# Kernel optimization log

Measured on AMD Instinct MI355X. Metric: run time of the kernel, lower is better.

## Reference

```python
import jax, jax.numpy as jnp
import numpy as np

N_NODES = 100000
N_EDGES = 1600000


def setup_inputs() -> dict:
    key = jax.random.key(0)
    ks = jax.random.split(key, 16)
    d_emb, d_mlp, d_lstm = 128, 256, 256
    B, C, T = 8, 4, 128
    return {
        "input_ids": jax.random.randint(ks[0], (B, C, T), 0, N_NODES, dtype=jnp.int64 if jax.config.jax_enable_x64 else jnp.int32),
        "input_mask": jnp.ones((B, C, T), dtype=jnp.int32),
        "labels": jax.random.uniform(ks[1], (B, C), dtype=jnp.float32),
        "src": jax.random.randint(ks[2], (N_EDGES,), 0, N_NODES),
        "dst": jax.random.randint(ks[3], (N_EDGES,), 0, N_NODES),
        "edge_value": jax.random.uniform(ks[4], (N_EDGES,), dtype=jnp.float32),
        "node_emb": jax.random.normal(ks[5], (N_NODES, d_emb), dtype=jnp.float32),
        "W1": jax.random.normal(ks[6], (d_mlp, d_emb), dtype=jnp.float32) * 0.05,
        "b1": jax.random.normal(ks[7], (d_mlp,), dtype=jnp.float32) * 0.05,
        "w_ih": jax.random.normal(ks[8], (4 * d_lstm, d_mlp), dtype=jnp.float32) * 0.05,
        "w_hh": jax.random.normal(ks[9], (4 * d_lstm, d_lstm), dtype=jnp.float32) * 0.05,
        "b_ih": jax.random.normal(ks[10], (4 * d_lstm,), dtype=jnp.float32) * 0.05,
        "b_hh": jax.random.normal(ks[11], (4 * d_lstm,), dtype=jnp.float32) * 0.05,
        "W2": jax.random.normal(ks[12], (1, d_lstm), dtype=jnp.float32) * 0.05,
        "b2": jax.random.normal(ks[13], (1,), dtype=jnp.float32) * 0.05,
    }


def reference(input_ids, input_mask, labels, src, dst, edge_value,
              node_emb, W1, b1, w_ih, w_hh, b_ih, b_hh, W2, b2):
    N = node_emb.shape[0]
    # edge-weighted mean message passing: u_mul_e('embedding','value') -> mean
    m = node_emb[src] * edge_value[:, None]                       # [E, d_emb]
    agg = jax.ops.segment_sum(m, dst, num_segments=N)             # [N, d_emb]
    cnt = jax.ops.segment_sum(jnp.ones_like(edge_value), dst, num_segments=N)
    h_nodes = agg / jnp.maximum(cnt, 1.0)[:, None]
    # linear1 on all nodes
    t_nodes = h_nodes @ W1.T + b1                                  # [N, d_mlp]
    B, C, T = input_ids.shape
    x = t_nodes[input_ids.reshape(B * C, T)]                       # [BC, T, d_mlp]
    lengths = input_mask.sum(axis=-1).reshape(B * C)               # [BC]
    H = w_hh.shape[1]

    def step(carry, xt):
        h, c = carry
        gates = xt @ w_ih.T + b_ih + h @ w_hh.T + b_hh
        i, f, g, o = jnp.split(gates, 4, axis=-1)  # torch LSTM gate order
        c = jax.nn.sigmoid(f) * c + jax.nn.sigmoid(i) * jnp.tanh(g)
        h = jax.nn.sigmoid(o) * jnp.tanh(c)
        return (h, c), h

    h0 = jnp.zeros((B * C, H), x.dtype)
    _, hs = jax.lax.scan(step, (h0, h0), jnp.swapaxes(x, 0, 1))    # [T, BC, H]
    hs = jnp.swapaxes(hs, 0, 1)                                    # [BC, T, H]
    idx = (lengths - 1).astype(jnp.int32)[:, None, None]
    h_last = jnp.take_along_axis(hs, jnp.broadcast_to(idx, (B * C, 1, H)), axis=1)[:, 0, :]
    scores = (h_last @ W2.T + b2).reshape(B, C)                    # [B, 4]
    p = jax.nn.softmax(scores, axis=1)
    # BCEWithLogits applied to softmaxed scores (as in the original)
    error = jnp.mean(jnp.maximum(p, 0) - p * labels + jnp.log1p(jnp.exp(-jnp.abs(p))))
    predictions = jnp.argmax(p, axis=1)
    return error, predictions
```

## Files before the change

### kernel.cpp

```cpp
#include <hip/hip_runtime.h>
#include <math.h>

#define NNODES 100000
#define NEDGES 1600000
#define NPOS   4096
#define NSEQ   32
#define TSTEPS 128

typedef float f32x4 __attribute__((ext_vector_type(4)));
typedef unsigned u32x4 __attribute__((ext_vector_type(4)));
typedef _Float16 h2v __attribute__((ext_vector_type(2)));

#define OFF_SLOT   0
#define OFF_AGG    400128
#define OFF_CNT    2497280
#define OFF_WF     2513664
#define OFF_BIASF  3037952
#define OFF_PREG   3042048
#define OFF_HS     19819264
#define OFF_WH16A  OFF_AGG
#define OFF_WH16L  (OFF_AGG + 192 * 512 * 4)

static __device__ __forceinline__ float fdot2(unsigned w, unsigned h, float acc) {
#if __has_builtin(__builtin_amdgcn_fdot2)
  h2v wv, hv;
  __builtin_memcpy(&wv, &w, 4);
  __builtin_memcpy(&hv, &h, 4);
  return __builtin_amdgcn_fdot2(wv, hv, acc, false);
#else
  asm("v_dot2_f32_f16 %0, %1, %2, %0" : "+v"(acc) : "v"(w), "v"(h));
  return acc;
#endif
}

__global__ void k_init(int* slotmap, float* agg, float* cnt, float* hs0) {
  int i = blockIdx.x * blockDim.x + threadIdx.x;
  int stride = gridDim.x * blockDim.x;
  for (int idx = i; idx < 4096 * 128; idx += stride) agg[idx] = 0.f;
  for (int idx = i; idx < NNODES; idx += stride) slotmap[idx] = -1;
  for (int idx = i; idx < 4096; idx += stride) cnt[idx] = 0.f;
  for (int idx = i; idx < 8192; idx += stride) hs0[idx] = 0.f;
}

__global__ void k_mark(const int* __restrict__ input_ids, int* __restrict__ slotmap) {
  int p = blockIdx.x * blockDim.x + threadIdx.x;
  if (p < NPOS) atomicCAS(&slotmap[input_ids[p]], -1, p);
}

__global__ void k_edge(const int* __restrict__ src, const int* __restrict__ dst,
                       const float* __restrict__ ev, const float* __restrict__ emb,
                       const int* __restrict__ slotmap,
                       float* __restrict__ agg, float* __restrict__ cnt) {
  int e = blockIdx.x * 256 + threadIdx.x;
  int lane = threadIdx.x & 63;
  int d = dst[e];
  int slot = slotmap[d];
  int sn = 0; float vv = 0.f;
  if (slot >= 0) { sn = src[e]; vv = ev[e]; }
  unsigned long long m = __ballot(slot >= 0);
  while (m) {
    int j = __ffsll(m) - 1;
    m &= m - 1;
    int sl = __shfl(slot, j);
    int s2 = __shfl(sn, j);
    float v = __shfl(vv, j);
    float2 em = *(const float2*)&emb[(size_t)s2 * 128 + 2 * lane];
    atomicAdd(&agg[sl * 128 + 2 * lane],     em.x * v);
    atomicAdd(&agg[sl * 128 + 2 * lane + 1], em.y * v);
    if (lane == 0) atomicAdd(&cnt[sl], 1.f);
  }
}

__global__ void k_div(float* __restrict__ agg, const float* __restrict__ cnt) {
  int i = blockIdx.x * blockDim.x + threadIdx.x;
  agg[i] /= fmaxf(cnt[i >> 7], 1.f);
}

__global__ void k_fuse(const float* __restrict__ w_ih, const float* __restrict__ W1,
                       const float* __restrict__ b1, const float* __restrict__ b_ih,
                       const float* __restrict__ b_hh,
                       float* __restrict__ Wf, float* __restrict__ bf) {
  int row = blockIdx.x;
  int e = threadIdx.x;
  float acc = 0.f;
  for (int m2 = 0; m2 < 256; ++m2) acc += w_ih[row * 256 + m2] * W1[m2 * 128 + e];
  Wf[row * 128 + e] = acc;
  if (e == 0) {
    float bacc = b_ih[row] + b_hh[row];
    for (int m2 = 0; m2 < 256; ++m2) bacc += w_ih[row * 256 + m2] * b1[m2];
    bf[row] = bacc;
  }
}

__global__ __launch_bounds__(256, 2) void k_pregemm(
    const float* __restrict__ hnode, const float* __restrict__ Wf,
    const float* __restrict__ bf, const int* __restrict__ slotmap,
    const int* __restrict__ input_ids, float* __restrict__ preg) {
  __shared__ float Ash[64][132];
  __shared__ float Bsh[64][132];
  __shared__ int slots[64];
  int tid = threadIdx.x;
  int bm = (blockIdx.x & 63) * 64;
  int bn = (blockIdx.x >> 6) * 64;
  if (tid < 64) slots[tid] = slotmap[input_ids[bm + tid]];
  __syncthreads();
#pragma unroll
  for (int i = 0; i < 8; ++i) {
    int idx = tid + 256 * i;
    int r = idx >> 5, c = idx & 31;
    *(float4*)&Ash[r][c * 4] = *(const float4*)&hnode[slots[r] * 128 + c * 4];
    *(float4*)&Bsh[r][c * 4] = *(const float4*)&Wf[(bn + r) * 128 + c * 4];
  }
  __syncthreads();
  int tx = tid & 15, ty = tid >> 4;
  float acc[4][4] = {};
  for (int k = 0; k < 128; k += 4) {
    float4 a[4], bb[4];
#pragma unroll
    for (int i = 0; i < 4; ++i) a[i] = *(const float4*)&Ash[tx + 16 * i][k];
#pragma unroll
    for (int j = 0; j < 4; ++j) bb[j] = *(const float4*)&Bsh[ty + 16 * j][k];
#pragma unroll
    for (int i = 0; i < 4; ++i)
#pragma unroll
      for (int j = 0; j < 4; ++j)
        acc[i][j] += a[i].x * bb[j].x + a[i].y * bb[j].y + a[i].z * bb[j].z + a[i].w * bb[j].w;
  }
#pragma unroll
  for (int j = 0; j < 4; ++j) {
    int row = bn + ty + 16 * j;
    float bias = bf[row];
    int q  = row >> 8;
    int mm = (row >> 5) & 7;
    int dl = row & 31;
#pragma unroll
    for (int i = 0; i < 4; ++i) {
      int p = bm + tx + 16 * i;
      int s = p >> 7, tt = p & 127;
      preg[(((size_t)(tt * 32 + s) * 8 + mm) * 4 + q) * 32 + dl] = acc[i][j] + bias;
    }
  }
}

__global__ void k_wcvt(const float* __restrict__ w_hh,
                       unsigned* __restrict__ wA, unsigned* __restrict__ wL) {
  int idx = blockIdx.x * 256 + threadIdx.x;
  int row = idx >> 7;
  int j   = idx & 127;
  float x0 = w_hh[(size_t)row * 256 + 2 * j];
  float x1 = w_hh[(size_t)row * 256 + 2 * j + 1];
  union { _Float16 f[2]; unsigned u; } pk;
  pk.f[0] = (_Float16)x0;
  pk.f[1] = (_Float16)x1;
  int q = row >> 8, d = row & 255;
  int kseg = j >> 6, jj = j & 63;
  int tid = kseg * 256 + d;
  if (q < 3) {
    wA[(q * 64 + jj) * 512 + tid] = pk.u;
  } else {
    wL[((jj >> 2) * 512 + tid) * 4 + (jj & 3)] = pk.u;
  }
}

__global__ __launch_bounds__(512) void k_lstm(
    const unsigned* __restrict__ wh16A, const unsigned* __restrict__ wh16L,
    const float* __restrict__ preg, float* __restrict__ hs) {
  __shared__ __align__(16) unsigned whL[16 * 512 * 4];
  __shared__ __align__(16) unsigned h16[128];
  __shared__ __align__(16) float    accb[256 * 4];
  const int tid  = threadIdx.x;
  const int s    = blockIdx.x;
  const int kseg = tid >> 8;
  const int d    = tid & 255;
  const bool owner = (kseg == 0);

  unsigned wv[192];
  {
    const unsigned* wa = wh16A + tid;
#pragma unroll
    for (int e = 0; e < 192; ++e) wv[e] = wa[e * 512];
#pragma unroll
    for (int i = 0; i < 16; ++i)
      *(u32x4*)&whL[(i * 512 + tid) * 4] = *(const u32x4*)&wh16L[(i * 512 + tid) * 4];
  }
  if (tid < 128) h16[tid] = 0u;
  float c_st = 0.f;
  __syncthreads();

  const float* pregs = preg + ((size_t)s * 8 + (d >> 5)) * 128 + (d & 31);

  for (int t = 0; t < TSTEPS; ++t) {
    float pg0 = 0.f, pg1 = 0.f, pg2 = 0.f, pg3 = 0.f;
    if (owner) {
      const float* pb = pregs + (size_t)t * 32768;
      pg0 = pb[0]; pg1 = pb[32]; pg2 = pb[64]; pg3 = pb[96];
    }
    float a0 = 0.f, a1 = 0.f, a2 = 0.f, a3 = 0.f;
    const unsigned* hseg = h16 + kseg * 64;
#pragma unroll
    for (int c = 0; c < 16; ++c) {
      u32x4 h4 = *(const u32x4*)(hseg + c * 4);
      u32x4 w3 = *(const u32x4*)&whL[(c * 512 + tid) * 4];
#pragma unroll
      for (int k = 0; k < 4; ++k) {
        a0 = fdot2(wv[0 * 64 + c * 4 + k], h4[k], a0);
        a1 = fdot2(wv[1 * 64 + c * 4 + k], h4[k], a1);
        a2 = fdot2(wv[2 * 64 + c * 4 + k], h4[k], a2);
        a3 = fdot2(w3[k],                  h4[k], a3);
      }
    }
    if (!owner) {
      f32x4 r; r.x = a0; r.y = a1; r.z = a2; r.w = a3;
      *(f32x4*)&accb[d * 4] = r;
    }
    __syncthreads();
    if (owner) {
      f32x4 r = *(const f32x4*)&accb[d * 4];
      float gi = a0 + r.x + pg0;
      float gf = a1 + r.y + pg1;
      float gg = a2 + r.z + pg2;
      float go = a3 + r.w + pg3;
      float si = 1.f / (1.f + expf(-gi));
      float sf = 1.f / (1.f + expf(-gf));
      float so = 1.f / (1.f + expf(-go));
      float cc = sf * c_st + si * tanhf(gg);
      float hh = so * tanhf(cc);
      c_st = cc;
      ((_Float16*)h16)[d] = (_Float16)hh;
      hs[(size_t)(t + 1) * 8192 + s * 256 + d] = hh;
    }
    __syncthreads();
  }
}

__global__ void k_final(const float* __restrict__ hs, const int* __restrict__ mask,
                        const float* __restrict__ labels, const float* __restrict__ W2,
                        const float* __restrict__ b2, float* __restrict__ out) {
  __shared__ float scores[32];
  __shared__ float errpart[8];
  int tid = threadIdx.x;
  if (tid < 32) {
    int len = 0;
    for (int t = 0; t < 128; ++t) len += mask[tid * 128 + t];
    if (len < 1) len = 1;
    const float* hl = hs + (size_t)len * 8192 + tid * 256;
    float acc = b2[0];
    for (int k = 0; k < 256; ++k) acc += hl[k] * W2[k];
    scores[tid] = acc;
  }
  __syncthreads();
  if (tid < 8) {
    float sc[4];
#pragma unroll
    for (int i = 0; i < 4; ++i) sc[i] = scores[tid * 4 + i];
    float mx = fmaxf(fmaxf(sc[0], sc[1]), fmaxf(sc[2], sc[3]));
    float ex[4], ssum = 0.f;
#pragma unroll
    for (int i = 0; i < 4; ++i) { ex[i] = expf(sc[i] - mx); ssum += ex[i]; }
    float esum = 0.f; int am = 0; float best = -1e30f;
#pragma unroll
    for (int i = 0; i < 4; ++i) {
      float p = ex[i] / ssum;
      float li = labels[tid * 4 + i];
      esum += fmaxf(p, 0.f) - p * li + log1pf(expf(-fabsf(p)));
      if (p > best) { best = p; am = i; }
    }
    errpart[tid] = esum;
    out[1 + tid] = (float)am;
  }
  __syncthreads();
  if (tid == 0) {
    float e = 0.f;
    for (int i = 0; i < 8; ++i) e += errpart[i];
    out[0] = e / 32.f;
  }
}

extern "C" void kernel_launch(void* const* d_in, const int* in_sizes, int n_in,
                              void* d_out, int out_size, void* d_ws, size_t ws_size,
                              hipStream_t stream) {
  const int*   input_ids  = (const int*)d_in[0];
  const int*   input_mask = (const int*)d_in[1];
  const float* labels     = (const float*)d_in[2];
  const int*   src        = (const int*)d_in[3];
  const int*   dst        = (const int*)d_in[4];
  const float* ev         = (const float*)d_in[5];
  const float* node_emb   = (const float*)d_in[6];
  const float* W1         = (const float*)d_in[7];
  const float* b1         = (const float*)d_in[8];
  const float* w_ih       = (const float*)d_in[9];
  const float* w_hh       = (const float*)d_in[10];
  const float* b_ih       = (const float*)d_in[11];
  const float* b_hh       = (const float*)d_in[12];
  const float* W2         = (const float*)d_in[13];
  const float* b2         = (const float*)d_in[14];
  float* out = (float*)d_out;
  char* ws = (char*)d_ws;
  int*      slotmap = (int*)(ws + OFF_SLOT);
  float*    agg     = (float*)(ws + OFF_AGG);
  float*    cnt     = (float*)(ws + OFF_CNT);
  float*    Wf      = (float*)(ws + OFF_WF);
  float*    biasf   = (float*)(ws + OFF_BIASF);
  float*    preg    = (float*)(ws + OFF_PREG);
  float*    hs      = (float*)(ws + OFF_HS);
  unsigned* wh16A   = (unsigned*)(ws + OFF_WH16A);
  unsigned* wh16L   = (unsigned*)(ws + OFF_WH16L);

  hipLaunchKernelGGL(k_init,    dim3(2048), dim3(256), 0, stream, slotmap, agg, cnt, hs);
  hipLaunchKernelGGL(k_mark,    dim3(16),   dim3(256), 0, stream, input_ids, slotmap);
  hipLaunchKernelGGL(k_edge,    dim3(6250), dim3(256), 0, stream, src, dst, ev, node_emb, slotmap, agg, cnt);
  hipLaunchKernelGGL(k_div,     dim3(2048), dim3(256), 0, stream, agg, cnt);
  hipLaunchKernelGGL(k_fuse,    dim3(1024), dim3(128), 0, stream, w_ih, W1, b1, b_ih, b_hh, Wf, biasf);
  hipLaunchKernelGGL(k_pregemm, dim3(1024), dim3(256), 0, stream, agg, Wf, biasf, slotmap, input_ids, preg);
  hipLaunchKernelGGL(k_wcvt,    dim3(512),  dim3(256), 0, stream, w_hh, wh16A, wh16L);
  hipLaunchKernelGGL(k_lstm,    dim3(NSEQ), dim3(512), 0, stream, wh16A, wh16L, preg, hs);
  hipLaunchKernelGGL(k_final,   dim3(1),    dim3(64),  0, stream, hs, input_mask, labels, W2, b2, out);
}
```

Measured before the change: 338.0 us.

## Repartition LSTM recurrence: two outputs per thread, four K-segments, weights split across registers/LDS/global

The recurrent LSTM kernel now has each thread compute gates for two hidden units over a quarter of the K dimension, instead of one unit over half of K. The fp16 w_hh is split three ways: a register-resident part (16 u32x4), an LDS part (18 chunks) and a part streamed from global/L2 each step (wS). The point is to cut per-step dot-product latency on the serial critical path and to spread the weight storage over the available storage levels. In exchange it adds global loads on every timestep, a three-way partial-sum reduction through LDS, and a complicated weight-layout conversion that could be wrong.

Result: slower. 381.0 us (+12.7%).

```diff
diff --git a/kernel.cpp b/kernel.cpp
--- a/kernel.cpp
+++ b/kernel.cpp
@@ -18,8 +18,9 @@
 #define OFF_BIASF  3037952
 #define OFF_PREG   3042048
 #define OFF_HS     19819264
-#define OFF_WH16A  OFF_AGG
-#define OFF_WH16L  (OFF_AGG + 192 * 512 * 4)
+#define OFF_WR  OFF_AGG
+#define OFF_WL  (OFF_AGG + 131072)
+#define OFF_WS  (OFF_AGG + 131072 + 147456)
 
 static __device__ __forceinline__ float fdot2(unsigned w, unsigned h, float acc) {
 #if __has_builtin(__builtin_amdgcn_fdot2)
@@ -31,6 +32,14 @@
   asm("v_dot2_f32_f16 %0, %1, %2, %0" : "+v"(acc) : "v"(w), "v"(h));
   return acc;
 #endif
+}
+
+static __device__ __forceinline__ float dotq(u32x4 w, u32x4 h, float a) {
+  a = fdot2(w[0], h[0], a);
+  a = fdot2(w[1], h[1], a);
+  a = fdot2(w[2], h[2], a);
+  a = fdot2(w[3], h[3], a);
+  return a;
 }
 
 __global__ void k_init(int* slotmap, float* agg, float* cnt, float* hs0) {
@@ -142,8 +151,8 @@
   }
 }
 
-__global__ void k_wcvt(const float* __restrict__ w_hh,
-                       unsigned* __restrict__ wA, unsigned* __restrict__ wL) {
+__global__ void k_wcvt(const float* __restrict__ w_hh, unsigned* __restrict__ wR,
+                       unsigned* __restrict__ wL, unsigned* __restrict__ wS) {
   int idx = blockIdx.x * 256 + threadIdx.x;
   int row = idx >> 7;
   int j   = idx & 127;
@@ -152,82 +161,153 @@
   union { _Float16 f[2]; unsigned u; } pk;
   pk.f[0] = (_Float16)x0;
   pk.f[1] = (_Float16)x1;
-  int q = row >> 8, d = row & 255;
-  int kseg = j >> 6, jj = j & 63;
-  int tid = kseg * 256 + d;
-  if (q < 3) {
-    wA[(q * 64 + jj) * 512 + tid] = pk.u;
+  int q = row >> 8, dout = row & 255;
+  int dim2 = dout & 1, dd2 = dout >> 1;
+  int r = dim2 * 4 + q;
+  int kseg = j >> 5, p = j & 31;
+  int b = p >> 4, i = (p >> 2) & 3, lane = p & 3;
+  int tid = kseg * 128 + dd2;
+  if (r < 2) {
+    int qr = (b * 2 + r) * 4 + i;
+    wR[(qr * 4 + lane) * 512 + tid] = pk.u;
+  } else if (b == 0 && (r == 3 || r == 4)) {
+    wL[(((r - 3) * 4 + i) * 512 + tid) * 4 + lane] = pk.u;
+  } else if (b == 1 && r == 2) {
+    wL[((8 + i) * 512 + tid) * 4 + lane] = pk.u;
+  } else if (b == 1 && r == 3) {
+    wL[((12 + i) * 512 + tid) * 4 + lane] = pk.u;
+  } else if (b == 1 && r == 4 && i < 2) {
+    wL[((16 + i) * 512 + tid) * 4 + lane] = pk.u;
+  } else if (b == 0 && r == 2) {
+    wS[(i * 512 + tid) * 4 + lane] = pk.u;
+  } else if (b == 0) {
+    wS[((4 + (r - 5) * 4 + i) * 512 + tid) * 4 + lane] = pk.u;
+  } else if (r == 4) {
+    wS[((16 + (i - 2)) * 512 + tid) * 4 + lane] = pk.u;
   } else {
-    wL[((jj >> 2) * 512 + tid) * 4 + (jj & 3)] = pk.u;
+    wS[((18 + (r - 5) * 4 + i) * 512 + tid) * 4 + lane] = pk.u;
   }
 }
 
 __global__ __launch_bounds__(512) void k_lstm(
-    const unsigned* __restrict__ wh16A, const unsigned* __restrict__ wh16L,
-    const float* __restrict__ preg, float* __restrict__ hs) {
-  __shared__ __align__(16) unsigned whL[16 * 512 * 4];
+    const unsigned* __restrict__ wR, const unsigned* __restrict__ wL,
+    const unsigned* __restrict__ wS, const float* __restrict__ preg,
+    float* __restrict__ hs) {
+  __shared__ __align__(16) unsigned whL[18 * 512 * 4];
   __shared__ __align__(16) unsigned h16[128];
-  __shared__ __align__(16) float    accb[256 * 4];
-  const int tid  = threadIdx.x;
-  const int s    = blockIdx.x;
-  const int kseg = tid >> 8;
-  const int d    = tid & 255;
+  __shared__ __align__(16) float    accb[3 * 128 * 8];
+  const int tid = threadIdx.x;
+  const int s = blockIdx.x;
+  const int kseg = tid >> 7;
+  const int dd2 = tid & 127;
   const bool owner = (kseg == 0);
 
-  unsigned wv[192];
+  u32x4 rq[16];
+#pragma unroll
+  for (int qr = 0; qr < 16; ++qr)
+#pragma unroll
+    for (int l = 0; l < 4; ++l)
+      rq[qr][l] = wR[(qr * 4 + l) * 512 + tid];
   {
-    const unsigned* wa = wh16A + tid;
-#pragma unroll
-    for (int e = 0; e < 192; ++e) wv[e] = wa[e * 512];
-#pragma unroll
-    for (int i = 0; i < 16; ++i)
-      *(u32x4*)&whL[(i * 512 + tid) * 4] = *(const u32x4*)&wh16L[(i * 512 + tid) * 4];
+    const u32x4* src = (const u32x4*)wL;
+    u32x4* dst = (u32x4*)whL;
+#pragma unroll
+    for (int lc = 0; lc < 18; ++lc)
+      dst[lc * 512 + tid] = src[lc * 512 + tid];
   }
   if (tid < 128) h16[tid] = 0u;
-  float c_st = 0.f;
-  __syncthreads();
-
-  const float* pregs = preg + ((size_t)s * 8 + (d >> 5)) * 128 + (d & 31);
+  float c0s = 0.f, c1s = 0.f;
+  __syncthreads();
+
+  const u32x4* hqp = (const u32x4*)h16 + kseg * 8;
+  const u32x4* lq = (const u32x4*)whL;
+  const u32x4* sq = (const u32x4*)wS;
 
   for (int t = 0; t < TSTEPS; ++t) {
-    float pg0 = 0.f, pg1 = 0.f, pg2 = 0.f, pg3 = 0.f;
+    float2 pg0, pg1, pg2, pg3;
     if (owner) {
-      const float* pb = pregs + (size_t)t * 32768;
-      pg0 = pb[0]; pg1 = pb[32]; pg2 = pb[64]; pg3 = pb[96];
+      const float* pb = preg + (((size_t)(t * 32 + s) * 8 + (dd2 >> 4)) * 4) * 32
+                        + ((2 * dd2) & 31);
+      pg0 = *(const float2*)&pb[0];
+      pg1 = *(const float2*)&pb[32];
+      pg2 = *(const float2*)&pb[64];
+      pg3 = *(const float2*)&pb[96];
     }
     float a0 = 0.f, a1 = 0.f, a2 = 0.f, a3 = 0.f;
-    const unsigned* hseg = h16 + kseg * 64;
-#pragma unroll
-    for (int c = 0; c < 16; ++c) {
-      u32x4 h4 = *(const u32x4*)(hseg + c * 4);
-      u32x4 w3 = *(const u32x4*)&whL[(c * 512 + tid) * 4];
-#pragma unroll
-      for (int k = 0; k < 4; ++k) {
-        a0 = fdot2(wv[0 * 64 + c * 4 + k], h4[k], a0);
-        a1 = fdot2(wv[1 * 64 + c * 4 + k], h4[k], a1);
-        a2 = fdot2(wv[2 * 64 + c * 4 + k], h4[k], a2);
-        a3 = fdot2(w3[k],                  h4[k], a3);
-      }
-    }
+    float a4 = 0.f, a5 = 0.f, a6 = 0.f, a7 = 0.f;
+    u32x4 A0 = sq[0 * 512 + tid], A1 = sq[1 * 512 + tid];
+    u32x4 A2 = sq[2 * 512 + tid], A3 = sq[3 * 512 + tid];
+    u32x4 B0 = sq[4 * 512 + tid], B1 = sq[5 * 512 + tid];
+    u32x4 B2 = sq[6 * 512 + tid], B3 = sq[7 * 512 + tid];
+    u32x4 h0 = hqp[0], h1 = hqp[1], h2 = hqp[2], h3 = hqp[3];
+    a0 = dotq(rq[3], h3, dotq(rq[2], h2, dotq(rq[1], h1, dotq(rq[0], h0, a0))));
+    a1 = dotq(rq[7], h3, dotq(rq[6], h2, dotq(rq[5], h1, dotq(rq[4], h0, a1))));
+    a2 = dotq(A3, h3, dotq(A2, h2, dotq(A1, h1, dotq(A0, h0, a2))));
+    u32x4 C0 = sq[8 * 512 + tid],  C1 = sq[9 * 512 + tid];
+    u32x4 C2 = sq[10 * 512 + tid], C3 = sq[11 * 512 + tid];
+    a3 = dotq(lq[3*512+tid], h3, dotq(lq[2*512+tid], h2,
+         dotq(lq[1*512+tid], h1, dotq(lq[0*512+tid], h0, a3))));
+    a4 = dotq(lq[7*512+tid], h3, dotq(lq[6*512+tid], h2,
+         dotq(lq[5*512+tid], h1, dotq(lq[4*512+tid], h0, a4))));
+    a5 = dotq(B3, h3, dotq(B2, h2, dotq(B1, h1, dotq(B0, h0, a5))));
+    u32x4 D0 = sq[12 * 512 + tid], D1 = sq[13 * 512 + tid];
+    u32x4 D2 = sq[14 * 512 + tid], D3 = sq[15 * 512 + tid];
+    a6 = dotq(C3, h3, dotq(C2, h2, dotq(C1, h1, dotq(C0, h0, a6))));
+    u32x4 E0 = sq[16 * 512 + tid], E1 = sq[17 * 512 + tid];
+    u32x4 E2 = sq[18 * 512 + tid], E3 = sq[19 * 512 + tid];
+    a7 = dotq(D3, h3, dotq(D2, h2, dotq(D1, h1, dotq(D0, h0, a7))));
+    h0 = hqp[4]; h1 = hqp[5]; h2 = hqp[6]; h3 = hqp[7];
+    u32x4 F0 = sq[20 * 512 + tid], F1 = sq[21 * 512 + tid];
+    u32x4 F2 = sq[22 * 512 + tid], F3 = sq[23 * 512 + tid];
+    a0 = dotq(rq[11], h3, dotq(rq[10], h2, dotq(rq[9], h1, dotq(rq[8], h0, a0))));
+    a1 = dotq(rq[15], h3, dotq(rq[14], h2, dotq(rq[13], h1, dotq(rq[12], h0, a1))));
+    u32x4 G0 = sq[24 * 512 + tid], G1 = sq[25 * 512 + tid];
+    u32x4 G2 = sq[26 * 512 + tid], G3 = sq[27 * 512 + tid];
+    a2 = dotq(lq[11*512+tid], h3, dotq(lq[10*512+tid], h2,
+         dotq(lq[9*512+tid], h1, dotq(lq[8*512+tid], h0, a2))));
+    u32x4 H0 = sq[28 * 512 + tid], H1 = sq[29 * 512 + tid];
+    a3 = dotq(lq[15*512+tid], h3, dotq(lq[14*512+tid], h2,
+         dotq(lq[13*512+tid], h1, dotq(lq[12*512+tid], h0, a3))));
+    a4 = dotq(E1, h3, dotq(E0, h2,
+         dotq(lq[17*512+tid], h1, dotq(lq[16*512+tid], h0, a4))));
+    a5 = dotq(F1, h3, dotq(F0, h2, dotq(E3, h1, dotq(E2, h0, a5))));
+    a6 = dotq(G1, h3, dotq(G0, h2, dotq(F3, h1, dotq(F2, h0, a6))));
+    a7 = dotq(H1, h3, dotq(H0, h2, dotq(G3, h1, dotq(G2, h0, a7))));
     if (!owner) {
-      f32x4 r; r.x = a0; r.y = a1; r.z = a2; r.w = a3;
-      *(f32x4*)&accb[d * 4] = r;
+      f32x4 pA; pA.x = a0; pA.y = a1; pA.z = a2; pA.w = a3;
+      f32x4 pB; pB.x = a4; pB.y = a5; pB.z = a6; pB.w = a7;
+      *(f32x4*)&accb[((kseg - 1) * 128 + dd2) * 8]     = pA;
+      *(f32x4*)&accb[((kseg - 1) * 128 + dd2) * 8 + 4] = pB;
     }
     __syncthreads();
     if (owner) {
-      f32x4 r = *(const f32x4*)&accb[d * 4];
-      float gi = a0 + r.x + pg0;
-      float gf = a1 + r.y + pg1;
-      float gg = a2 + r.z + pg2;
-      float go = a3 + r.w + pg3;
-      float si = 1.f / (1.f + expf(-gi));
-      float sf = 1.f / (1.f + expf(-gf));
-      float so = 1.f / (1.f + expf(-go));
-      float cc = sf * c_st + si * tanhf(gg);
-      float hh = so * tanhf(cc);
-      c_st = cc;
-      ((_Float16*)h16)[d] = (_Float16)hh;
-      hs[(size_t)(t + 1) * 8192 + s * 256 + d] = hh;
+#pragma unroll
+      for (int ks = 0; ks < 3; ++ks) {
+        f32x4 pA = *(const f32x4*)&accb[(ks * 128 + dd2) * 8];
+        f32x4 pB = *(const f32x4*)&accb[(ks * 128 + dd2) * 8 + 4];
+        a0 += pA.x; a1 += pA.y; a2 += pA.z; a3 += pA.w;
+        a4 += pB.x; a5 += pB.y; a6 += pB.z; a7 += pB.w;
+      }
+      float gi0 = a0 + pg0.x, gf0 = a1 + pg1.x, gg0 = a2 + pg2.x, go0 = a3 + pg3.x;
+      float gi1 = a4 + pg0.y, gf1 = a5 + pg1.y, gg1 = a6 + pg2.y, go1 = a7 + pg3.y;
+      float si0 = 1.f / (1.f + expf(-gi0));
+      float sf0 = 1.f / (1.f + expf(-gf0));
+      float so0 = 1.f / (1.f + expf(-go0));
+      float cc0 = sf0 * c0s + si0 * tanhf(gg0);
+      float hh0 = so0 * tanhf(cc0);
+      c0s = cc0;
+      float si1 = 1.f / (1.f + expf(-gi1));
+      float sf1 = 1.f / (1.f + expf(-gf1));
+      float so1 = 1.f / (1.f + expf(-go1));
+      float cc1 = sf1 * c1s + si1 * tanhf(gg1);
+      float hh1 = so1 * tanhf(cc1);
+      c1s = cc1;
+      union { _Float16 f[2]; unsigned u; } hp;
+      hp.f[0] = (_Float16)hh0;
+      hp.f[1] = (_Float16)hh1;
+      h16[dd2] = hp.u;
+      float2 hv; hv.x = hh0; hv.y = hh1;
+      *(float2*)&hs[(size_t)(t + 1) * 8192 + s * 256 + 2 * dd2] = hv;
     }
     __syncthreads();
   }
@@ -303,8 +383,9 @@
   float*    biasf   = (float*)(ws + OFF_BIASF);
   float*    preg    = (float*)(ws + OFF_PREG);
   float*    hs      = (float*)(ws + OFF_HS);
-  unsigned* wh16A   = (unsigned*)(ws + OFF_WH16A);
-  unsigned* wh16L   = (unsigned*)(ws + OFF_WH16L);
+  unsigned* wRimg   = (unsigned*)(ws + OFF_WR);
+  unsigned* wLimg   = (unsigned*)(ws + OFF_WL);
+  unsigned* wSimg   = (unsigned*)(ws + OFF_WS);
 
   hipLaunchKernelGGL(k_init,    dim3(2048), dim3(256), 0, stream, slotmap, agg, cnt, hs);
   hipLaunchKernelGGL(k_mark,    dim3(16),   dim3(256), 0, stream, input_ids, slotmap);
@@ -312,7 +393,7 @@
   hipLaunchKernelGGL(k_div,     dim3(2048), dim3(256), 0, stream, agg, cnt);
   hipLaunchKernelGGL(k_fuse,    dim3(1024), dim3(128), 0, stream, w_ih, W1, b1, b_ih, b_hh, Wf, biasf);
   hipLaunchKernelGGL(k_pregemm, dim3(1024), dim3(256), 0, stream, agg, Wf, biasf, slotmap, input_ids, preg);
-  hipLaunchKernelGGL(k_wcvt,    dim3(512),  dim3(256), 0, stream, w_hh, wh16A, wh16L);
-  hipLaunchKernelGGL(k_lstm,    dim3(NSEQ), dim3(512), 0, stream, wh16A, wh16L, preg, hs);
+  hipLaunchKernelGGL(k_wcvt,    dim3(512),  dim3(256), 0, stream, w_hh, wRimg, wLimg, wSimg);
+  hipLaunchKernelGGL(k_lstm,    dim3(NSEQ), dim3(512), 0, stream, wRimg, wLimg, wSimg, preg, hs);
   hipLaunchKernelGGL(k_final,   dim3(1),    dim3(64),  0, stream, hs, input_mask, labels, W2, b2, out);
 }
```
